# Kernel tuning notes

Hardware: AMD Instinct MI355X
Metric: run time of the kernel (lower is better)

## Reference

```python
import jax, jax.numpy as jnp
import numpy as np

N = 50000
E = 800000
DIM = 256
H = 8
HD = DIM // H


def setup_inputs() -> dict:
    key = jax.random.key(0)
    ks = jax.random.split(key, 8)
    s = 0.02
    return {
        "x": jax.random.normal(ks[0], (N, DIM), jnp.float32),
        "src": jax.random.randint(ks[1], (E,), 0, N, jnp.int32),
        "dst": jax.random.randint(ks[2], (E,), 0, N, jnp.int32),
        "Wqkv": jax.random.normal(ks[3], (DIM, 3 * DIM), jnp.float32) * s,
        "bqkv": jnp.zeros((3 * DIM,), jnp.float32),
        "Wout": jax.random.normal(ks[4], (DIM, DIM), jnp.float32) * s,
        "bout": jnp.zeros((DIM,), jnp.float32),
        "W1": jax.random.normal(ks[5], (2 * DIM, DIM), jnpp := jnp.float32) * s,
        "b1": jnp.zeros((DIM,), jnp.float32),
        "W2": jax.random.normal(ks[6], (DIM, DIM), jnp.float32) * s,
        "b2": jnp.zeros((DIM,), jnp.float32),
    }


def reference(x, src, dst, Wqkv, bqkv, Wout, bout, W1, b1, W2, b2):
    n = x.shape[0]
    scale = 1.0 / np.sqrt(HD).astype(np.float32)
    # QKV projection; torch reshapes [N, 3*dim] -> [N, H, 3*hd] then splits per head
    qkv = (x @ Wqkv + bqkv).reshape(n, H, 3 * HD)
    q, k, v = qkv[..., :HD], qkv[..., HD:2 * HD], qkv[..., 2 * HD:]
    # per-edge attention scores: key at src dotted with query at dst -> [E, H]
    scores = jnp.einsum('ehd,ehd->eh', k[src], q[dst]) * scale
    # edge softmax grouped by destination node
    m = jax.ops.segment_max(scores, dst, num_segments=n)  # [N, H]
    p = jnp.exp(scores - m[dst])
    denom = jax.ops.segment_sum(p, dst, num_segments=n)  # [N, H]
    probs = p / denom[dst]
    # weighted scatter-sum aggregation of source values -> [N, H, HD]
    agg = jax.ops.segment_sum(v[src] * probs[..., None], dst, num_segments=n)
    agg = agg.reshape(n, DIM) @ Wout + bout
    # feed-forward over concat([x, aggregated])
    h = jnp.concatenate([x, agg], axis=1)
    h = jax.nn.gelu(h @ W1 + b1, approximate=False)
    return h @ W2 + b2
```

## Files before the change

kernel.cpp:

```cpp
#include <hip/hip_runtime.h>
#include <hip/hip_bf16.h>
#include <math.h>

#define NDIM 256
#define HDIM 32
#define SCB 512

typedef __attribute__((ext_vector_type(8))) short bf16x8;
typedef __attribute__((ext_vector_type(4))) float f32x4;
typedef __attribute__((ext_vector_type(2))) float f32x2;
typedef unsigned long long ull;

__device__ inline float bf2f(unsigned short u) {
  union { unsigned int i; float f; } c; c.i = ((unsigned int)u) << 16; return c.f;
}
__device__ inline unsigned short f2bf(float f) {
  union { float f; unsigned int i; } c; c.f = f;
  unsigned int x = c.i;
  unsigned int lsb = (x >> 16) & 1u;
  x += 0x7fffu + lsb;
  return (unsigned short)(x >> 16);
}
__device__ inline float4 ldbf4(const unsigned short* p) {
  ull raw = *(const ull*)p;
  float4 f;
  f.x = bf2f((unsigned short)(raw));
  f.y = bf2f((unsigned short)(raw >> 16));
  f.z = bf2f((unsigned short)(raw >> 32));
  f.w = bf2f((unsigned short)(raw >> 48));
  return f;
}
__device__ inline void stbf4(unsigned short* p, float4 v) {
  ull raw = (ull)f2bf(v.x) | ((ull)f2bf(v.y) << 16)
          | ((ull)f2bf(v.z) << 32) | ((ull)f2bf(v.w) << 48);
  *(ull*)p = raw;
}
__device__ inline ull pk4_bf16(float v0, float v1, float v2, float v3) {
  return (ull)f2bf(v0) | ((ull)f2bf(v1) << 16) | ((ull)f2bf(v2) << 32) | ((ull)f2bf(v3) << 48);
}

__device__ inline unsigned char f2e4m3(float v) {
#if __has_builtin(__builtin_amdgcn_cvt_pk_fp8_f32)
  return (unsigned char)(__builtin_amdgcn_cvt_pk_fp8_f32(v, v, 0, false) & 0xff);
#else
  union { float f; unsigned int u; } c; c.f = v;
  unsigned char s = (unsigned char)((c.u >> 24) & 0x80);
  float a = fabsf(v);
  if (!(a < 448.f)) return (unsigned char)(s | 0x7e);
  if (a < 0.0009765625f) return s;
  int e = (int)((c.u >> 23) & 0xff) - 127;
  if (e < -6) {
    int q = (int)rintf(ldexpf(a, 9));
    if (q >= 8) return (unsigned char)(s | 0x08);
    return (unsigned char)(s | q);
  }
  int q = (int)rintf(ldexpf(a, 3 - e));
  if (q == 16) { e++; q = 8; }
  if (e > 8) return (unsigned char)(s | 0x7e);
  return (unsigned char)(s | ((e + 7) << 3) | (q - 8));
#endif
}
__device__ inline unsigned int pk4_e4m3(float v0, float v1, float v2, float v3) {
#if __has_builtin(__builtin_amdgcn_cvt_pk_fp8_f32)
  int w = __builtin_amdgcn_cvt_pk_fp8_f32(v0, v1, 0, false);
  w = __builtin_amdgcn_cvt_pk_fp8_f32(v2, v3, w, true);
  return (unsigned int)w;
#else
  return (unsigned int)f2e4m3(v0) | ((unsigned int)f2e4m3(v1) << 8)
       | ((unsigned int)f2e4m3(v2) << 16) | ((unsigned int)f2e4m3(v3) << 24);
#endif
}
template<bool HI>
__device__ inline f32x2 e4m3pk(unsigned int w) {
#if __has_builtin(__builtin_amdgcn_cvt_pk_f32_fp8)
  return __builtin_amdgcn_cvt_pk_f32_fp8((int)w, HI);
#else
  unsigned int h = HI ? (w >> 16) : w;
  f32x2 r;
  #pragma unroll
  for (int j = 0; j < 2; ++j) {
    unsigned char b = (unsigned char)(h >> (8 * j));
    int e = (b >> 3) & 0xf, mm = b & 7;
    float val = e ? ldexpf((float)(8 + mm), e - 10) : ldexpf((float)mm, -9);
    r[j] = (b & 0x80) ? -val : val;
  }
  return r;
#endif
}

__global__ void fuse0_k(
    const float* __restrict__ x, unsigned short* __restrict__ xb, int n8, int nbx,
    const float* __restrict__ Wqkv, unsigned short* __restrict__ wqkvt,
    const float* __restrict__ W1, unsigned short* __restrict__ wf,
    const float* __restrict__ W2, unsigned short* __restrict__ w2t,
    const float* __restrict__ Wout, const float* __restrict__ bout,
    const float* __restrict__ b1, float* __restrict__ bc, int nbw,
    const int* __restrict__ dst, int* __restrict__ deg, int* __restrict__ erank, int E)
{
  int b = blockIdx.x;
  int tid = threadIdx.x;
  if (b < nbx) {
    int i = b * 256 + tid;
    if (i < n8) {
      const float* p = x + (size_t)i * 8;
      float4 a = *(const float4*)p;
      float4 bv = *(const float4*)(p + 4);
      ull lo = (ull)f2bf(a.x) | ((ull)f2bf(a.y) << 16) | ((ull)f2bf(a.z) << 32) | ((ull)f2bf(a.w) << 48);
      ull hi = (ull)f2bf(bv.x) | ((ull)f2bf(bv.y) << 16) | ((ull)f2bf(bv.z) << 32) | ((ull)f2bf(bv.w) << 48);
      ull* d = (ull*)(xb + (size_t)i * 8);
      d[0] = lo; d[1] = hi;
    }
    return;
  }
  b -= nbx;
  if (b < nbw) {
    int idx = b * 256 + tid;
    if (idx < 196608) {
      int j = idx >> 8, k = idx & 255;
      int seg = j >> 8, jj = j & 255;
      int h = jj >> 5, t = jj & 31;
      int orig = h * 96 + seg * 32 + t;
      wqkvt[(size_t)j * 256 + k] = f2bf(Wqkv[(size_t)k * 768 + orig]);
    } else if (idx < 262144) {
      int i2 = idx - 196608;
      int n = i2 >> 8, k = i2 & 255;
      wf[(size_t)n * 512 + k] = f2bf(W1[(size_t)k * 256 + n]);
    } else if (idx < 327680) {
      int i3 = idx - 262144;
      int n = i3 >> 8, k = i3 & 255;
      w2t[(size_t)n * 256 + k] = f2bf(W2[(size_t)k * 256 + n]);
    } else if (idx < 393216) {
      int i4 = idx - 327680;
      int a = i4 >> 8, n = i4 & 255;
      float s = 0.f;
      #pragma unroll 4
      for (int j = 0; j < 256; ++j)
        s += Wout[(size_t)a * 256 + j] * W1[(size_t)(256 + j) * 256 + n];
      wf[(size_t)n * 512 + 256 + a] = f2bf(s);
    } else if (idx < 393472) {
      int n = idx - 393216;
      float s = b1[n];
      for (int j = 0; j < 256; ++j)
        s += bout[j] * W1[(size_t)(256 + j) * 256 + n];
      bc[n] = s;
    }
    return;
  }
  b -= nbw;
  int e = b * 256 + tid;
  if (e < E) {
    int r = atomicAdd(&deg[dst[e]], 1);
    erank[e] = r;
  }
}

__global__ __launch_bounds__(SCB) void bsum_k(const int* __restrict__ deg, int* __restrict__ bsum, int n) {
  int tid = threadIdx.x;
  int i = blockIdx.x * SCB + tid;
  int v = (i < n) ? deg[i] : 0;
  #pragma unroll
  for (int d = 1; d < 64; d <<= 1) v += __shfl_xor(v, d);
  __shared__ int wsum[8];
  if ((tid & 63) == 0) wsum[tid >> 6] = v;
  __syncthreads();
  if (tid == 0) {
    int s = 0;
    #pragma unroll
    for (int j = 0; j < 8; ++j) s += wsum[j];
    bsum[blockIdx.x] = s;
  }
}

__global__ __launch_bounds__(128) void bscan_k(int* __restrict__ bsum, int nb) {
  __shared__ int tmp[128];
  int tid = threadIdx.x;
  int v = (tid < nb) ? bsum[tid] : 0;
  tmp[tid] = v;
  __syncthreads();
  for (int d = 1; d < 128; d <<= 1) {
    int t = (tid >= d) ? tmp[tid - d] : 0;
    __syncthreads();
    tmp[tid] += t;
    __syncthreads();
  }
  if (tid < nb) bsum[tid] = tmp[tid];
}

__global__ __launch_bounds__(SCB) void offs_k(const int* __restrict__ deg, const int* __restrict__ bsum,
                                              int* __restrict__ offs, int n) {
  int tid = threadIdx.x, lane = tid & 63, wid = tid >> 6;
  int b = blockIdx.x;
  int i = b * SCB + tid;
  int v = (i < n) ? deg[i] : 0;
  int incl = v;
  #pragma unroll
  for (int d = 1; d < 64; d <<= 1) { int t = __shfl_up(incl, d); if (lane >= d) incl += t; }
  __shared__ int wsum[8];
  if (lane == 63) wsum[wid] = incl;
  __syncthreads();
  if (tid < 8) {
    int s = wsum[tid];
    #pragma unroll
    for (int d = 1; d < 8; d <<= 1) { int t = __shfl_up(s, d); if (tid >= d) s += t; }
    wsum[tid] = s;
  }
  __syncthreads();
  int base = (b > 0 ? bsum[b - 1] : 0) + (wid > 0 ? wsum[wid - 1] : 0);
  if (i < n) offs[i] = base + incl - v;
  if (i == n - 1) offs[n] = base + incl;
}

__global__ void scatter2_k(const int* __restrict__ src, const int* __restrict__ dstv,
                           const int* __restrict__ offs, const int* __restrict__ erank,
                           int* __restrict__ ssrc, int E) {
  int e = blockIdx.x * 256 + threadIdx.x;
  if (e < E) ssrc[offs[dstv[e]] + erank[e]] = src[e];
}

__global__ __launch_bounds__(256) void attn_k(
    const unsigned short* Q,
    const unsigned char* __restrict__ K8,
    const unsigned char* __restrict__ V8,
    const int* __restrict__ offs,
    const int* __restrict__ ssrc,
    unsigned short* agg, int N)
{
  int n = blockIdx.x * 4 + (threadIdx.x >> 6);
  if (n >= N) return;
  int lane = threadIdx.x & 63;
  int col = lane << 2;
  const float scale = 0.17677669529663689f;
  float4 q4 = ldbf4(Q + (size_t)n * NDIM + col);
  q4.x *= scale; q4.y *= scale; q4.z *= scale; q4.w *= scale;
  int e0 = offs[n], e1 = offs[n + 1];
  float den = 0.f;
  float ax = 0.f, ay = 0.f, az = 0.f, aw = 0.f;
  int e = e0;
  for (; e + 8 <= e1; e += 8) {
    unsigned int kw[8], vw[8];
    #pragma unroll
    for (int j = 0; j < 8; ++j) {
      int s = ssrc[e + j];
      kw[j] = *(const unsigned int*)(K8 + (size_t)s * NDIM + col);
      vw[j] = *(const unsigned int*)(V8 + (size_t)s * NDIM + col);
    }
    float d[8];
    #pragma unroll
    for (int j = 0; j < 8; ++j) {
      f32x2 k01 = e4m3pk<false>(kw[j]);
      f32x2 k23 = e4m3pk<true>(kw[j]);
      d[j] = q4.x * k01[0] + q4.y * k01[1] + q4.z * k23[0] + q4.w * k23[1];
    }
    #pragma unroll
    for (int j = 0; j < 8; ++j) {
      d[j] += __shfl_xor(d[j], 1);
      d[j] += __shfl_xor(d[j], 2);
      d[j] += __shfl_xor(d[j], 4);
    }
    #pragma unroll
    for (int j = 0; j < 8; ++j) {
      float p = __expf(d[j]);
      den += p;
      f32x2 v01 = e4m3pk<false>(vw[j]);
      f32x2 v23 = e4m3pk<true>(vw[j]);
      ax += p * v01[0]; ay += p * v01[1];
      az += p * v23[0]; aw += p * v23[1];
    }
  }
  for (; e + 4 <= e1; e += 4) {
    unsigned int kw[4], vw[4];
    #pragma unroll
    for (int j = 0; j < 4; ++j) {
      int s = ssrc[e + j];
      kw[j] = *(const unsigned int*)(K8 + (size_t)s * NDIM + col);
      vw[j] = *(const unsigned int*)(V8 + (size_t)s * NDIM + col);
    }
    float d[4];
    #pragma unroll
    for (int j = 0; j < 4; ++j) {
      f32x2 k01 = e4m3pk<false>(kw[j]);
      f32x2 k23 = e4m3pk<true>(kw[j]);
      d[j] = q4.x * k01[0] + q4.y * k01[1] + q4.z * k23[0] + q4.w * k23[1];
    }
    #pragma unroll
    for (int j = 0; j < 4; ++j) {
      d[j] += __shfl_xor(d[j], 1);
      d[j] += __shfl_xor(d[j], 2);
      d[j] += __shfl_xor(d[j], 4);
    }
    #pragma unroll
    for (int j = 0; j < 4; ++j) {
      float p = __expf(d[j]);
      den += p;
      f32x2 v01 = e4m3pk<false>(vw[j]);
      f32x2 v23 = e4m3pk<true>(vw[j]);
      ax += p * v01[0]; ay += p * v01[1];
      az += p * v23[0]; aw += p * v23[1];
    }
  }
  for (; e < e1; ++e) {
    int s = ssrc[e];
    unsigned int kw = *(const unsigned int*)(K8 + (size_t)s * NDIM + col);
    unsigned int vw = *(const unsigned int*)(V8 + (size_t)s * NDIM + col);
    f32x2 k01 = e4m3pk<false>(kw);
    f32x2 k23 = e4m3pk<true>(kw);
    float d = q4.x * k01[0] + q4.y * k01[1] + q4.z * k23[0] + q4.w * k23[1];
    d += __shfl_xor(d, 1);
    d += __shfl_xor(d, 2);
    d += __shfl_xor(d, 4);
    float p = __expf(d);
    den += p;
    f32x2 v01 = e4m3pk<false>(vw);
    f32x2 v23 = e4m3pk<true>(vw);
    ax += p * v01[0]; ay += p * v01[1];
    az += p * v23[0]; aw += p * v23[1];
  }
  float inv = (den > 0.f) ? 1.f / den : 0.f;
  stbf4(agg + (size_t)n * NDIM + col, make_float4(ax * inv, ay * inv, az * inv, aw * inv));
}

__global__ __launch_bounds__(256, 4) void qkv_k(
    const unsigned short* __restrict__ A1, const unsigned short* __restrict__ Wt,
    const float* __restrict__ bias,
    unsigned short* __restrict__ Oq, unsigned char* __restrict__ Ok, unsigned char* __restrict__ Ov,
    int M)
{
  __shared__ char smem[32768];
  unsigned short* As = (unsigned short*)smem;
  unsigned short* Bs = (unsigned short*)(smem + 16384);
  const int tid = threadIdx.x;
  const int lane = tid & 63;
  const int wid = tid >> 6;

  const int nwg = gridDim.x;
  const int q8 = nwg >> 3, r8 = nwg & 7;
  const int xcd = blockIdx.x & 7, idx8 = blockIdx.x >> 3;
  const int swz = (xcd < r8 ? xcd * (q8 + 1) : r8 * (q8 + 1) + (xcd - r8) * q8) + idx8;
  const int nct = 6;
  const int bmt = swz / nct;
  const int bnt = swz - bmt * nct;
  const int bm = bmt * 128;
  const int bn = bnt * 128;

  const int wr = (wid >> 1) << 6;
  const int wc = (wid & 1) << 6;
  const int l15 = lane & 15, lhi = lane >> 4;
  const int srow = lane >> 3;
  const int ssl = (((lane & 7) ^ (lane >> 3)) << 3);

  f32x4 acc[4][4];
  #pragma unroll
  for (int i = 0; i < 4; ++i)
    #pragma unroll
    for (int j = 0; j < 4; ++j) acc[i][j] = (f32x4){0.f, 0.f, 0.f, 0.f};

  for (int k0 = 0; k0 < 256; k0 += 64) {
    #pragma unroll
    for (int t = 0; t < 4; ++t) {
      int qi = wid * 4 + t;
      const unsigned short* ga = A1 + (size_t)(bm + qi * 8 + srow) * 256 + k0 + ssl;
      __builtin_amdgcn_global_load_lds(
          (const __attribute__((address_space(1))) void*)ga,
          (__attribute__((address_space(3))) void*)&As[qi * 512], 16, 0, 0);
      const unsigned short* gb = Wt + (size_t)(bn + qi * 8 + srow) * 256 + k0 + ssl;
      __builtin_amdgcn_global_load_lds(
          (const __attribute__((address_space(1))) void*)gb,
          (__attribute__((address_space(3))) void*)&Bs[qi * 512], 16, 0, 0);
    }
    __syncthreads();
    #pragma unroll
    for (int kk = 0; kk < 64; kk += 32) {
      bf16x8 af[4], bfr[4];
      #pragma unroll
      for (int mi = 0; mi < 4; ++mi) {
        int rA = wr + mi * 16 + l15;
        af[mi] = *(const bf16x8*)&As[rA * 64 + ((((kk >> 3) + lhi) ^ (rA & 7)) << 3)];
      }
      #pragma unroll
      for (int ni = 0; ni < 4; ++ni) {
        int rB = wc + ni * 16 + l15;
        bfr[ni] = *(const bf16x8*)&Bs[rB * 64 + ((((kk >> 3) + lhi) ^ (rB & 7)) << 3)];
      }
      #pragma unroll
      for (int mi = 0; mi < 4; ++mi)
        #pragma unroll
        for (int ni = 0; ni < 4; ++ni)
          acc[mi][ni] = __builtin_amdgcn_mfma_f32_16x16x32_bf16(bfr[ni], af[mi], acc[mi][ni], 0, 0, 0);
    }
    __syncthreads();
  }

  const int seg = (bn + wc) >> 8;
  const int jjbase = (bn + wc) & 255;
  char* slabB = smem + wid * 8192;
  if (seg == 0) {
    #pragma unroll
    for (int ni = 0; ni < 4; ++ni) {
      int cl = ni * 16 + (lhi << 2);
      int jj = jjbase + cl;
      float4 bb = *(const float4*)&bias[(jj >> 5) * 96 + (jj & 31)];
      #pragma unroll
      for (int mi = 0; mi < 4; ++mi) {
        int rl = mi * 16 + l15;
        *(ull*)&slabB[rl * 128 + ((cl * 2) ^ ((rl & 7) << 4))] = pk4_bf16(
            acc[mi][ni][0] + bb.x, acc[mi][ni][1] + bb.y,
            acc[mi][ni][2] + bb.z, acc[mi][ni][3] + bb.w);
      }
    }
    asm volatile("s_waitcnt lgkmcnt(0)" ::: "memory");
    __builtin_amdgcn_sched_barrier(0);
    int rl0 = lane >> 3, co = (lane & 7) << 4;
    #pragma unroll
    for (int t = 0; t < 8; ++t) {
      int rl = t * 8 + rl0;
      int gr = bm + wr + rl;
      if (gr < M)
        *(float4*)&Oq[(size_t)gr * NDIM + jjbase + (co >> 1)] =
            *(float4*)&slabB[rl * 128 + (co ^ ((rl & 7) << 4))];
    }
  } else {
    unsigned char* dstp = (seg == 1) ? Ok : Ov;
    #pragma unroll
    for (int ni = 0; ni < 4; ++ni) {
      int cl = ni * 16 + (lhi << 2);
      int jj = jjbase + cl;
      float4 bb = *(const float4*)&bias[(jj >> 5) * 96 + seg * 32 + (jj & 31)];
      #pragma unroll
      for (int mi = 0; mi < 4; ++mi) {
        int rl = mi * 16 + l15;
        *(unsigned int*)&slabB[rl * 64 + (cl ^ ((rl & 3) << 4))] = pk4_e4m3(
            acc[mi][ni][0] + bb.x, acc[mi][ni][1] + bb.y,
            acc[mi][ni][2] + bb.z, acc[mi][ni][3] + bb.w);
      }
    }
    asm volatile("s_waitcnt lgkmcnt(0)" ::: "memory");
    __builtin_amdgcn_sched_barrier(0);
    int rl0 = lane >> 2, co = (lane & 3) << 4;
    #pragma unroll
    for (int t = 0; t < 4; ++t) {
      int rl = t * 16 + rl0;
      int gr = bm + wr + rl;
      if (gr < M)
        *(float4*)&dstp[(size_t)gr * NDIM + jjbase + co] =
            *(float4*)&slabB[rl * 64 + (co ^ ((rl & 3) << 4))];
    }
  }
}

template<int EPI>
__global__ __launch_bounds__(256, 4) void mgemm_k(
    const unsigned short* __restrict__ A1, const unsigned short* __restrict__ A2,
    const unsigned short* __restrict__ Wt, const float* __restrict__ bias,
    float* __restrict__ Cf, unsigned short* __restrict__ Cb,
    int M, int K1, int K, int Ncol, int ldb, int nct)
{
  __shared__ char smem[32768];
  unsigned short* As = (unsigned short*)smem;
  unsigned short* Bs = (unsigned short*)(smem + 16384);
  const int tid = threadIdx.x;
  const int lane = tid & 63;
  const int wid = tid >> 6;

  const int nwg = gridDim.x;
  const int q8 = nwg >> 3, r8 = nwg & 7;
  const int xcd = blockIdx.x & 7, idx8 = blockIdx.x >> 3;
  const int swz = (xcd < r8 ? xcd * (q8 + 1) : r8 * (q8 + 1) + (xcd - r8) * q8) + idx8;
  const int bmt = swz / nct;
  const int bnt = swz - bmt * nct;
  const int bm = bmt * 128;
  const int bn = bnt * 128;

  const int wr = (wid >> 1) << 6;
  const int wc = (wid & 1) << 6;
  const int l15 = lane & 15, lhi = lane >> 4;
  const int srow = lane >> 3;
  const int ssl = (((lane & 7) ^ (lane >> 3)) << 3);

  f32x4 acc[4][4];
  #pragma unroll
  for (int i = 0; i < 4; ++i)
    #pragma unroll
    for (int j = 0; j < 4; ++j) acc[i][j] = (f32x4){0.f, 0.f, 0.f, 0.f};

  for (int k0 = 0; k0 < K; k0 += 64) {
    const unsigned short* Ab;
    int ks;
    if (k0 < K1) { Ab = A1; ks = k0; } else { Ab = A2; ks = k0 - K1; }
    #pragma unroll
    for (int t = 0; t < 4; ++t) {
      int qi = wid * 4 + t;
      const unsigned short* ga = Ab + (size_t)(bm + qi * 8 + srow) * 256 + ks + ssl;
      __builtin_amdgcn_global_load_lds(
          (const __attribute__((address_space(1))) void*)ga,
          (__attribute__((address_space(3))) void*)&As[qi * 512], 16, 0, 0);
      const unsigned short* gb = Wt + (size_t)(bn + qi * 8 + srow) * ldb + k0 + ssl;
      __builtin_amdgcn_global_load_lds(
          (const __attribute__((address_space(1))) void*)gb,
          (__attribute__((address_space(3))) void*)&Bs[qi * 512], 16, 0, 0);
    }
    __syncthreads();
    #pragma unroll
    for (int kk = 0; kk < 64; kk += 32) {
      bf16x8 af[4], bfr[4];
      #pragma unroll
      for (int mi = 0; mi < 4; ++mi) {
        int rA = wr + mi * 16 + l15;
        af[mi] = *(const bf16x8*)&As[rA * 64 + ((((kk >> 3) + lhi) ^ (rA & 7)) << 3)];
      }
      #pragma unroll
      for (int ni = 0; ni < 4; ++ni) {
        int rB = wc + ni * 16 + l15;
        bfr[ni] = *(const bf16x8*)&Bs[rB * 64 + ((((kk >> 3) + lhi) ^ (rB & 7)) << 3)];
      }
      #pragma unroll
      for (int mi = 0; mi < 4; ++mi)
        #pragma unroll
        for (int ni = 0; ni < 4; ++ni)
          acc[mi][ni] = __builtin_amdgcn_mfma_f32_16x16x32_bf16(bfr[ni], af[mi], acc[mi][ni], 0, 0, 0);
    }
    __syncthreads();
  }

  char* slabB = smem + wid * 8192;
  if (EPI == 0) {
    #pragma unroll
    for (int half = 0; half < 2; ++half) {
      #pragma unroll
      for (int nj = 0; nj < 2; ++nj) {
        int ni = half * 2 + nj;
        int cl = nj * 16 + (lhi << 2);
        float4 bb = *(const float4*)&bias[bn + wc + half * 32 + cl];
        #pragma unroll
        for (int mi = 0; mi < 4; ++mi) {
          int rl = mi * 16 + l15;
          *(float4*)&slabB[rl * 128 + ((cl * 4) ^ ((rl & 7) << 4))] = make_float4(
              acc[mi][ni][0] + bb.x, acc[mi][ni][1] + bb.y,
              acc[mi][ni][2] + bb.z, acc[mi][ni][3] + bb.w);
        }
      }
      asm volatile("s_waitcnt lgkmcnt(0)" ::: "memory");
      __builtin_amdgcn_sched_barrier(0);
      int rl0 = lane >> 3, co = (lane & 7) << 4;
      #pragma unroll
      for (int t = 0; t < 8; ++t) {
        int rl = t * 8 + rl0;
        int gr = bm + wr + rl;
        if (gr < M)
          *(float4*)&Cf[(size_t)gr * Ncol + bn + wc + half * 32 + (co >> 2)] =
              *(float4*)&slabB[rl * 128 + (co ^ ((rl & 7) << 4))];
      }
      if (half == 0) {
        asm volatile("s_waitcnt lgkmcnt(0)" ::: "memory");
        __builtin_amdgcn_sched_barrier(0);
      }
    }
  } else {
    #pragma unroll
    for (int ni = 0; ni < 4; ++ni) {
      int cl = ni * 16 + (lhi << 2);
      float4 bb = *(const float4*)&bias[bn + wc + cl];
      #pragma unroll
      for (int mi = 0; mi < 4; ++mi) {
        int rl = mi * 16 + l15;
        float v0 = acc[mi][ni][0] + bb.x;
        float v1 = acc[mi][ni][1] + bb.y;
        float v2 = acc[mi][ni][2] + bb.z;
        float v3 = acc[mi][ni][3] + bb.w;
        v0 = 0.5f * v0 * (1.0f + erff(v0 * 0.70710678118654752f));
        v1 = 0.5f * v1 * (1.0f + erff(v1 * 0.70710678118654752f));
        v2 = 0.5f * v2 * (1.0f + erff(v2 * 0.70710678118654752f));
        v3 = 0.5f * v3 * (1.0f + erff(v3 * 0.70710678118654752f));
        *(ull*)&slabB[rl * 128 + ((cl * 2) ^ ((rl & 7) << 4))] = pk4_bf16(v0, v1, v2, v3);
      }
    }
    asm volatile("s_waitcnt lgkmcnt(0)" ::: "memory");
    __builtin_amdgcn_sched_barrier(0);
    int rl0 = lane >> 3, co = (lane & 7) << 4;
    #pragma unroll
    for (int t = 0; t < 8; ++t) {
      int rl = t * 8 + rl0;
      int gr = bm + wr + rl;
      if (gr < M)
        *(float4*)&Cb[(size_t)gr * Ncol + bn + wc + (co >> 1)] =
            *(float4*)&slabB[rl * 128 + (co ^ ((rl & 7) << 4))];
    }
  }
}

extern "C" void kernel_launch(void* const* d_in, const int* in_sizes, int n_in,
                              void* d_out, int out_size, void* d_ws, size_t ws_size,
                              hipStream_t stream) {
  (void)n_in; (void)out_size; (void)ws_size;
  const float* x    = (const float*)d_in[0];
  const int*   src  = (const int*)d_in[1];
  const int*   dst  = (const int*)d_in[2];
  const float* Wqkv = (const float*)d_in[3];
  const float* bqkv = (const float*)d_in[4];
  const float* Wout = (const float*)d_in[5];
  const float* bout = (const float*)d_in[6];
  const float* W1   = (const float*)d_in[7];
  const float* b1   = (const float*)d_in[8];
  const float* W2   = (const float*)d_in[9];
  const float* b2   = (const float*)d_in[10];
  float* out = (float*)d_out;

  const int N = in_sizes[0] / NDIM;
  const int E = in_sizes[1];
  const int Mp = (N + 127) & ~127;
  const int nb = (N + SCB - 1) / SCB;

  char* ws = (char*)d_ws;
  size_t off = 0;
  auto alloc = [&](size_t bytes) -> char* {
    char* p = ws + off;
    off += (bytes + 255) & ~(size_t)255;
    return p;
  };
  unsigned short* xb   = (unsigned short*)alloc((size_t)Mp * NDIM * 2);
  unsigned short* Q    = (unsigned short*)alloc((size_t)Mp * NDIM * 2);
  unsigned short* Kb   = (unsigned short*)alloc((size_t)Mp * NDIM * 2);
  unsigned short* Vb   = (unsigned short*)alloc((size_t)Mp * NDIM * 2);
  unsigned short* wqkvt = (unsigned short*)alloc((size_t)768 * 256 * 2);
  unsigned short* wft   = (unsigned short*)alloc((size_t)256 * 512 * 2);
  unsigned short* w2t   = (unsigned short*)alloc((size_t)256 * 256 * 2);
  float*          bc    = (float*)alloc(256 * 4);
  int* deg    = (int*)alloc((size_t)N * 4);
  int* offs   = (int*)alloc((size_t)(N + 1) * 4);
  int* erank  = (int*)alloc((size_t)E * 4);
  int* ssrc   = (int*)alloc((size_t)E * 4);
  int* bsum   = (int*)alloc((size_t)nb * 4);

  unsigned char* K8 = (unsigned char*)Kb;
  unsigned char* V8 = (unsigned char*)Vb;
  unsigned short* agg = Q;
  unsigned short* h1  = Kb;

  const int n8  = N * NDIM / 8;
  const int nbx = (n8 + 255) / 256;
  const int nbw = (393472 + 255) / 256;
  const int nsc = (E + 255) / 256;
  const int mt  = Mp / 128;

  hipMemsetAsync(deg, 0, (size_t)N * 4, stream);

  fuse0_k<<<nbx + nbw + nsc, 256, 0, stream>>>(
      x, xb, n8, nbx, Wqkv, wqkvt, W1, wft, W2, w2t, Wout, bout, b1, bc, nbw,
      dst, deg, erank, E);

  bsum_k<<<nb, SCB, 0, stream>>>(deg, bsum, N);
  bscan_k<<<1, 128, 0, stream>>>(bsum, nb);
  offs_k<<<nb, SCB, 0, stream>>>(deg, bsum, offs, N);

  scatter2_k<<<nsc, 256, 0, stream>>>(src, dst, offs, erank, ssrc, E);

  qkv_k<<<mt * 6, 256, 0, stream>>>(xb, wqkvt, bqkv, Q, K8, V8, N);

  attn_k<<<(N + 3) / 4, 256, 0, stream>>>(Q, K8, V8, offs, ssrc, agg, N);

  mgemm_k<2><<<mt * 2, 256, 0, stream>>>(
      xb, agg, wft, bc, nullptr, h1, N, 256, 512, 256, 512, 2);

  mgemm_k<0><<<mt * 2, 256, 0, stream>>>(
      h1, nullptr, w2t, b2, out, nullptr, N, 256, 256, 256, 256, 2);
}
```

Baseline: 220.8 us.

## Fuse degree histogram into QKV GEMM launch and interleave K/V rows

Moves the edge-degree histogram out of the prep kernel and into the QKV GEMM launch as extra blocks, so the atomic histogram runs alongside the GEMM tiles. K and V fp8 outputs are stored interleaved in one 512-byte row per node, so attention fetches K and V for a source node from the same row. Edge ranks are narrowed to 16-bit to halve that buffer, and the GEMM launch bounds are raised to five waves per SIMD. This risks overflow if any node's in-degree exceeds 65535, and may spill registers under the tighter occupancy bound.

```diff
diff --git a/kernel.cpp b/kernel.cpp
--- a/kernel.cpp
+++ b/kernel.cpp
@@ -3,7 +3,6 @@
 #include <math.h>
 
 #define NDIM 256
-#define HDIM 32
 #define SCB 512
 
 typedef __attribute__((ext_vector_type(8))) short bf16x8;
@@ -88,14 +87,13 @@
 #endif
 }
 
-__global__ void fuse0_k(
+__global__ void prep_k(
     const float* __restrict__ x, unsigned short* __restrict__ xb, int n8, int nbx,
     const float* __restrict__ Wqkv, unsigned short* __restrict__ wqkvt,
     const float* __restrict__ W1, unsigned short* __restrict__ wf,
     const float* __restrict__ W2, unsigned short* __restrict__ w2t,
     const float* __restrict__ Wout, const float* __restrict__ bout,
-    const float* __restrict__ b1, float* __restrict__ bc, int nbw,
-    const int* __restrict__ dst, int* __restrict__ deg, int* __restrict__ erank, int E)
+    const float* __restrict__ b1, float* __restrict__ bc)
 {
   int b = blockIdx.x;
   int tid = threadIdx.x;
@@ -113,44 +111,173 @@
     return;
   }
   b -= nbx;
-  if (b < nbw) {
-    int idx = b * 256 + tid;
-    if (idx < 196608) {
-      int j = idx >> 8, k = idx & 255;
-      int seg = j >> 8, jj = j & 255;
-      int h = jj >> 5, t = jj & 31;
-      int orig = h * 96 + seg * 32 + t;
-      wqkvt[(size_t)j * 256 + k] = f2bf(Wqkv[(size_t)k * 768 + orig]);
-    } else if (idx < 262144) {
-      int i2 = idx - 196608;
-      int n = i2 >> 8, k = i2 & 255;
-      wf[(size_t)n * 512 + k] = f2bf(W1[(size_t)k * 256 + n]);
-    } else if (idx < 327680) {
-      int i3 = idx - 262144;
-      int n = i3 >> 8, k = i3 & 255;
-      w2t[(size_t)n * 256 + k] = f2bf(W2[(size_t)k * 256 + n]);
-    } else if (idx < 393216) {
-      int i4 = idx - 327680;
-      int a = i4 >> 8, n = i4 & 255;
-      float s = 0.f;
-      #pragma unroll 4
-      for (int j = 0; j < 256; ++j)
-        s += Wout[(size_t)a * 256 + j] * W1[(size_t)(256 + j) * 256 + n];
-      wf[(size_t)n * 512 + 256 + a] = f2bf(s);
-    } else if (idx < 393472) {
-      int n = idx - 393216;
-      float s = b1[n];
-      for (int j = 0; j < 256; ++j)
-        s += bout[j] * W1[(size_t)(256 + j) * 256 + n];
-      bc[n] = s;
+  int idx = b * 256 + tid;
+  if (idx < 196608) {
+    int j = idx >> 8, k = idx & 255;
+    int seg = j >> 8, jj = j & 255;
+    int h = jj >> 5, t = jj & 31;
+    int orig = h * 96 + seg * 32 + t;
+    wqkvt[(size_t)j * 256 + k] = f2bf(Wqkv[(size_t)k * 768 + orig]);
+  } else if (idx < 262144) {
+    int i2 = idx - 196608;
+    int n = i2 >> 8, k = i2 & 255;
+    wf[(size_t)n * 512 + k] = f2bf(W1[(size_t)k * 256 + n]);
+  } else if (idx < 327680) {
+    int i3 = idx - 262144;
+    int n = i3 >> 8, k = i3 & 255;
+    w2t[(size_t)n * 256 + k] = f2bf(W2[(size_t)k * 256 + n]);
+  } else if (idx < 393216) {
+    int i4 = idx - 327680;
+    int a = i4 >> 8, n = i4 & 255;
+    float s = 0.f;
+    #pragma unroll 4
+    for (int j = 0; j < 256; ++j)
+      s += Wout[(size_t)a * 256 + j] * W1[(size_t)(256 + j) * 256 + n];
+    wf[(size_t)n * 512 + 256 + a] = f2bf(s);
+  } else if (idx < 393472) {
+    int n = idx - 393216;
+    float s = b1[n];
+    for (int j = 0; j < 256; ++j)
+      s += bout[j] * W1[(size_t)(256 + j) * 256 + n];
+    bc[n] = s;
+  }
+}
+
+__global__ __launch_bounds__(256, 5) void histqkv_k(
+    const int* __restrict__ dstv, int* __restrict__ deg,
+    unsigned short* __restrict__ erank, int E, int nhist,
+    const unsigned short* __restrict__ A1, const unsigned short* __restrict__ Wt,
+    const float* __restrict__ bias,
+    unsigned short* __restrict__ Oq, unsigned char* __restrict__ KV,
+    int M)
+{
+  __shared__ char smem[32768];
+  if (blockIdx.x < nhist) {
+    int e = blockIdx.x * 256 + threadIdx.x;
+    if (e < E) {
+      int r = atomicAdd(&deg[dstv[e]], 1);
+      erank[e] = (unsigned short)r;
     }
     return;
   }
-  b -= nbw;
-  int e = b * 256 + tid;
-  if (e < E) {
-    int r = atomicAdd(&deg[dst[e]], 1);
-    erank[e] = r;
+  unsigned short* As = (unsigned short*)smem;
+  unsigned short* Bs = (unsigned short*)(smem + 16384);
+  const int tid = threadIdx.x;
+  const int lane = tid & 63;
+  const int wid = tid >> 6;
+
+  const int nwg = gridDim.x - nhist;
+  const int bid = blockIdx.x - nhist;
+  const int q8 = nwg >> 3, r8 = nwg & 7;
+  const int xcd = bid & 7, idx8 = bid >> 3;
+  const int swz = (xcd < r8 ? xcd * (q8 + 1) : r8 * (q8 + 1) + (xcd - r8) * q8) + idx8;
+  const int bmt = swz / 6;
+  const int bnt = swz - bmt * 6;
+  const int bm = bmt * 128;
+  const int bn = bnt * 128;
+
+  const int wr = (wid >> 1) << 6;
+  const int wc = (wid & 1) << 6;
+  const int l15 = lane & 15, lhi = lane >> 4;
+  const int srow = lane >> 3;
+  const int ssl = (((lane & 7) ^ (lane >> 3)) << 3);
+
+  f32x4 acc[4][4];
+  #pragma unroll
+  for (int i = 0; i < 4; ++i)
+    #pragma unroll
+    for (int j = 0; j < 4; ++j) acc[i][j] = (f32x4){0.f, 0.f, 0.f, 0.f};
+
+  for (int k0 = 0; k0 < 256; k0 += 64) {
+    #pragma unroll
+    for (int t = 0; t < 4; ++t) {
+      int qi = wid * 4 + t;
+      const unsigned short* ga = A1 + (size_t)(bm + qi * 8 + srow) * 256 + k0 + ssl;
+      __builtin_amdgcn_global_load_lds(
+          (const __attribute__((address_space(1))) void*)ga,
+          (__attribute__((address_space(3))) void*)&As[qi * 512], 16, 0, 0);
+      const unsigned short* gb = Wt + (size_t)(bn + qi * 8 + srow) * 256 + k0 + ssl;
+      __builtin_amdgcn_global_load_lds(
+          (const __attribute__((address_space(1))) void*)gb,
+          (__attribute__((address_space(3))) void*)&Bs[qi * 512], 16, 0, 0);
+    }
+    __syncthreads();
+    #pragma unroll
+    for (int kk = 0; kk < 64; kk += 32) {
+      bf16x8 af[4], bfr[4];
+      #pragma unroll
+      for (int mi = 0; mi < 4; ++mi) {
+        int rA = wr + mi * 16 + l15;
+        af[mi] = *(const bf16x8*)&As[rA * 64 + ((((kk >> 3) + lhi) ^ (rA & 7)) << 3)];
+      }
+      #pragma unroll
+      for (int ni = 0; ni < 4; ++ni) {
+        int rB = wc + ni * 16 + l15;
+        bfr[ni] = *(const bf16x8*)&Bs[rB * 64 + ((((kk >> 3) + lhi) ^ (rB & 7)) << 3)];
+      }
+      #pragma unroll
+      for (int mi = 0; mi < 4; ++mi)
+        #pragma unroll
+        for (int ni = 0; ni < 4; ++ni)
+          acc[mi][ni] = __builtin_amdgcn_mfma_f32_16x16x32_bf16(bfr[ni], af[mi], acc[mi][ni], 0, 0, 0);
+    }
+    __syncthreads();
+  }
+
+  const int seg = (bn + wc) >> 8;
+  const int jjbase = (bn + wc) & 255;
+  char* slabB = smem + wid * 8192;
+  if (seg == 0) {
+    #pragma unroll
+    for (int ni = 0; ni < 4; ++ni) {
+      int cl = ni * 16 + (lhi << 2);
+      int jj = jjbase + cl;
+      float4 bb = *(const float4*)&bias[(jj >> 5) * 96 + (jj & 31)];
+      #pragma unroll
+      for (int mi = 0; mi < 4; ++mi) {
+        int rl = mi * 16 + l15;
+        *(ull*)&slabB[rl * 128 + ((cl * 2) ^ ((rl & 7) << 4))] = pk4_bf16(
+            acc[mi][ni][0] + bb.x, acc[mi][ni][1] + bb.y,
+            acc[mi][ni][2] + bb.z, acc[mi][ni][3] + bb.w);
+      }
+    }
+    asm volatile("s_waitcnt lgkmcnt(0)" ::: "memory");
+    __builtin_amdgcn_sched_barrier(0);
+    int rl0 = lane >> 3, co = (lane & 7) << 4;
+    #pragma unroll
+    for (int t = 0; t < 8; ++t) {
+      int rl = t * 8 + rl0;
+      int gr = bm + wr + rl;
+      if (gr < M)
+        *(float4*)&Oq[(size_t)gr * NDIM + jjbase + (co >> 1)] =
+            *(float4*)&slabB[rl * 128 + (co ^ ((rl & 7) << 4))];
+    }
+  } else {
+    unsigned char* dstp = KV + ((seg == 1) ? 0 : 256);
+    #pragma unroll
+    for (int ni = 0; ni < 4; ++ni) {
+      int cl = ni * 16 + (lhi << 2);
+      int jj = jjbase + cl;
+      float4 bb = *(const float4*)&bias[(jj >> 5) * 96 + seg * 32 + (jj & 31)];
+      #pragma unroll
+      for (int mi = 0; mi < 4; ++mi) {
+        int rl = mi * 16 + l15;
+        *(unsigned int*)&slabB[rl * 64 + (cl ^ ((rl & 3) << 4))] = pk4_e4m3(
+            acc[mi][ni][0] + bb.x, acc[mi][ni][1] + bb.y,
+            acc[mi][ni][2] + bb.z, acc[mi][ni][3] + bb.w);
+      }
+    }
+    asm volatile("s_waitcnt lgkmcnt(0)" ::: "memory");
+    __builtin_amdgcn_sched_barrier(0);
+    int rl0 = lane >> 2, co = (lane & 3) << 4;
+    #pragma unroll
+    for (int t = 0; t < 4; ++t) {
+      int rl = t * 16 + rl0;
+      int gr = bm + wr + rl;
+      if (gr < M)
+        *(float4*)&dstp[(size_t)gr * 512 + jjbase + co] =
+            *(float4*)&slabB[rl * 64 + (co ^ ((rl & 3) << 4))];
+    }
   }
 }
 
@@ -211,7 +338,7 @@
 }
 
 __global__ void scatter2_k(const int* __restrict__ src, const int* __restrict__ dstv,
-                           const int* __restrict__ offs, const int* __restrict__ erank,
+                           const int* __restrict__ offs, const unsigned short* __restrict__ erank,
                            int* __restrict__ ssrc, int E) {
   int e = blockIdx.x * 256 + threadIdx.x;
   if (e < E) ssrc[offs[dstv[e]] + erank[e]] = src[e];
@@ -219,8 +346,7 @@
 
 __global__ __launch_bounds__(256) void attn_k(
     const unsigned short* Q,
-    const unsigned char* __restrict__ K8,
-    const unsigned char* __restrict__ V8,
+    const unsigned char* __restrict__ KV,
     const int* __restrict__ offs,
     const int* __restrict__ ssrc,
     unsigned short* agg, int N)
@@ -241,8 +367,9 @@
     #pragma unroll
     for (int j = 0; j < 8; ++j) {
       int s = ssrc[e + j];
-      kw[j] = *(const unsigned int*)(K8 + (size_t)s * NDIM + col);
-      vw[j] = *(const unsigned int*)(V8 + (size_t)s * NDIM + col);
+      const unsigned char* row = KV + (size_t)s * 512 + col;
+      kw[j] = *(const unsigned int*)row;
+      vw[j] = *(const unsigned int*)(row + 256);
     }
     float d[8];
     #pragma unroll
@@ -272,8 +399,9 @@
     #pragma unroll
     for (int j = 0; j < 4; ++j) {
       int s = ssrc[e + j];
-      kw[j] = *(const unsigned int*)(K8 + (size_t)s * NDIM + col);
-      vw[j] = *(const unsigned int*)(V8 + (size_t)s * NDIM + col);
+      const unsigned char* row = KV + (size_t)s * 512 + col;
+      kw[j] = *(const unsigned int*)row;
+      vw[j] = *(const unsigned int*)(row + 256);
     }
     float d[4];
     #pragma unroll
@@ -300,8 +428,9 @@
   }
   for (; e < e1; ++e) {
     int s = ssrc[e];
-    unsigned int kw = *(const unsigned int*)(K8 + (size_t)s * NDIM + col);
-    unsigned int vw = *(const unsigned int*)(V8 + (size_t)s * NDIM + col);
+    const unsigned char* row = KV + (size_t)s * 512 + col;
+    unsigned int kw = *(const unsigned int*)row;
+    unsigned int vw = *(const unsigned int*)(row + 256);
     f32x2 k01 = e4m3pk<false>(kw);
     f32x2 k23 = e4m3pk<true>(kw);
     float d = q4.x * k01[0] + q4.y * k01[1] + q4.z * k23[0] + q4.w * k23[1];
@@ -319,136 +448,8 @@
   stbf4(agg + (size_t)n * NDIM + col, make_float4(ax * inv, ay * inv, az * inv, aw * inv));
 }
 
-__global__ __launch_bounds__(256, 4) void qkv_k(
-    const unsigned short* __restrict__ A1, const unsigned short* __restrict__ Wt,
-    const float* __restrict__ bias,
-    unsigned short* __restrict__ Oq, unsigned char* __restrict__ Ok, unsigned char* __restrict__ Ov,
-    int M)
-{
-  __shared__ char smem[32768];
-  unsigned short* As = (unsigned short*)smem;
-  unsigned short* Bs = (unsigned short*)(smem + 16384);
-  const int tid = threadIdx.x;
-  const int lane = tid & 63;
-  const int wid = tid >> 6;
-
-  const int nwg = gridDim.x;
-  const int q8 = nwg >> 3, r8 = nwg & 7;
-  const int xcd = blockIdx.x & 7, idx8 = blockIdx.x >> 3;
-  const int swz = (xcd < r8 ? xcd * (q8 + 1) : r8 * (q8 + 1) + (xcd - r8) * q8) + idx8;
-  const int nct = 6;
-  const int bmt = swz / nct;
-  const int bnt = swz - bmt * nct;
-  const int bm = bmt * 128;
-  const int bn = bnt * 128;
-
-  const int wr = (wid >> 1) << 6;
-  const int wc = (wid & 1) << 6;
-  const int l15 = lane & 15, lhi = lane >> 4;
-  const int srow = lane >> 3;
-  const int ssl = (((lane & 7) ^ (lane >> 3)) << 3);
-
-  f32x4 acc[4][4];
-  #pragma unroll
-  for (int i = 0; i < 4; ++i)
-    #pragma unroll
-    for (int j = 0; j < 4; ++j) acc[i][j] = (f32x4){0.f, 0.f, 0.f, 0.f};
-
-  for (int k0 = 0; k0 < 256; k0 += 64) {
-    #pragma unroll
-    for (int t = 0; t < 4; ++t) {
-      int qi = wid * 4 + t;
-      const unsigned short* ga = A1 + (size_t)(bm + qi * 8 + srow) * 256 + k0 + ssl;
-      __builtin_amdgcn_global_load_lds(
-          (const __attribute__((address_space(1))) void*)ga,
-          (__attribute__((address_space(3))) void*)&As[qi * 512], 16, 0, 0);
-      const unsigned short* gb = Wt + (size_t)(bn + qi * 8 + srow) * 256 + k0 + ssl;
-      __builtin_amdgcn_global_load_lds(
-          (const __attribute__((address_space(1))) void*)gb,
-          (__attribute__((address_space(3))) void*)&Bs[qi * 512], 16, 0, 0);
-    }
-    __syncthreads();
-    #pragma unroll
-    for (int kk = 0; kk < 64; kk += 32) {
-      bf16x8 af[4], bfr[4];
-      #pragma unroll
-      for (int mi = 0; mi < 4; ++mi) {
-        int rA = wr + mi * 16 + l15;
-        af[mi] = *(const bf16x8*)&As[rA * 64 + ((((kk >> 3) + lhi) ^ (rA & 7)) << 3)];
-      }
-      #pragma unroll
-      for (int ni = 0; ni < 4; ++ni) {
-        int rB = wc + ni * 16 + l15;
-        bfr[ni] = *(const bf16x8*)&Bs[rB * 64 + ((((kk >> 3) + lhi) ^ (rB & 7)) << 3)];
-      }
-      #pragma unroll
-      for (int mi = 0; mi < 4; ++mi)
-        #pragma unroll
-        for (int ni = 0; ni < 4; ++ni)
-          acc[mi][ni] = __builtin_amdgcn_mfma_f32_16x16x32_bf16(bfr[ni], af[mi], acc[mi][ni], 0, 0, 0);
-    }
-    __syncthreads();
-  }
-
-  const int seg = (bn + wc) >> 8;
-  const int jjbase = (bn + wc) & 255;
-  char* slabB = smem + wid * 8192;
-  if (seg == 0) {
-    #pragma unroll
-    for (int ni = 0; ni < 4; ++ni) {
-      int cl = ni * 16 + (lhi << 2);
-      int jj = jjbase + cl;
-      float4 bb = *(const float4*)&bias[(jj >> 5) * 96 + (jj & 31)];
-      #pragma unroll
-      for (int mi = 0; mi < 4; ++mi) {
-        int rl = mi * 16 + l15;
-        *(ull*)&slabB[rl * 128 + ((cl * 2) ^ ((rl & 7) << 4))] = pk4_bf16(
-            acc[mi][ni][0] + bb.x, acc[mi][ni][1] + bb.y,
-            acc[mi][ni][2] + bb.z, acc[mi][ni][3] + bb.w);
-      }
-    }
-    asm volatile("s_waitcnt lgkmcnt(0)" ::: "memory");
-    __builtin_amdgcn_sched_barrier(0);
-    int rl0 = lane >> 3, co = (lane & 7) << 4;
-    #pragma unroll
-    for (int t = 0; t < 8; ++t) {
-      int rl = t * 8 + rl0;
-      int gr = bm + wr + rl;
-      if (gr < M)
-        *(float4*)&Oq[(size_t)gr * NDIM + jjbase + (co >> 1)] =
-            *(float4*)&slabB[rl * 128 + (co ^ ((rl & 7) << 4))];
-    }
-  } else {
-    unsigned char* dstp = (seg == 1) ? Ok : Ov;
-    #pragma unroll
-    for (int ni = 0; ni < 4; ++ni) {
-      int cl = ni * 16 + (lhi << 2);
-      int jj = jjbase + cl;
-      float4 bb = *(const float4*)&bias[(jj >> 5) * 96 + seg * 32 + (jj & 31)];
-      #pragma unroll
-      for (int mi = 0; mi < 4; ++mi) {
-        int rl = mi * 16 + l15;
-        *(unsigned int*)&slabB[rl * 64 + (cl ^ ((rl & 3) << 4))] = pk4_e4m3(
-            acc[mi][ni][0] + bb.x, acc[mi][ni][1] + bb.y,
-            acc[mi][ni][2] + bb.z, acc[mi][ni][3] + bb.w);
-      }
-    }
-    asm volatile("s_waitcnt lgkmcnt(0)" ::: "memory");
-    __builtin_amdgcn_sched_barrier(0);
-    int rl0 = lane >> 2, co = (lane & 3) << 4;
-    #pragma unroll
-    for (int t = 0; t < 4; ++t) {
-      int rl = t * 16 + rl0;
-      int gr = bm + wr + rl;
-      if (gr < M)
-        *(float4*)&dstp[(size_t)gr * NDIM + jjbase + co] =
-            *(float4*)&slabB[rl * 64 + (co ^ ((rl & 3) << 4))];
-    }
-  }
-}
-
 template<int EPI>
-__global__ __launch_bounds__(256, 4) void mgemm_k(
+__global__ __launch_bounds__(256, 5) void mgemm_k(
     const unsigned short* __restrict__ A1, const unsigned short* __restrict__ A2,
     const unsigned short* __restrict__ Wt, const float* __restrict__ bias,
     float* __restrict__ Cf, unsigned short* __restrict__ Cb,
@@ -618,22 +619,19 @@
   };
   unsigned short* xb   = (unsigned short*)alloc((size_t)Mp * NDIM * 2);
   unsigned short* Q    = (unsigned short*)alloc((size_t)Mp * NDIM * 2);
-  unsigned short* Kb   = (unsigned short*)alloc((size_t)Mp * NDIM * 2);
-  unsigned short* Vb   = (unsigned short*)alloc((size_t)Mp * NDIM * 2);
+  unsigned char*  KV   = (unsigned char*)alloc((size_t)Mp * 512);
+  unsigned short* h1   = (unsigned short*)alloc((size_t)Mp * NDIM * 2);
   unsigned short* wqkvt = (unsigned short*)alloc((size_t)768 * 256 * 2);
   unsigned short* wft   = (unsigned short*)alloc((size_t)256 * 512 * 2);
   unsigned short* w2t   = (unsigned short*)alloc((size_t)256 * 256 * 2);
   float*          bc    = (float*)alloc(256 * 4);
   int* deg    = (int*)alloc((size_t)N * 4);
   int* offs   = (int*)alloc((size_t)(N + 1) * 4);
-  int* erank  = (int*)alloc((size_t)E * 4);
+  unsigned short* erank = (unsigned short*)alloc((size_t)E * 2);
   int* ssrc   = (int*)alloc((size_t)E * 4);
   int* bsum   = (int*)alloc((size_t)nb * 4);
 
-  unsigned char* K8 = (unsigned char*)Kb;
-  unsigned char* V8 = (unsigned char*)Vb;
   unsigned short* agg = Q;
-  unsigned short* h1  = Kb;
 
   const int n8  = N * NDIM / 8;
   const int nbx = (n8 + 255) / 256;
@@ -643,9 +641,12 @@
 
   hipMemsetAsync(deg, 0, (size_t)N * 4, stream);
 
-  fuse0_k<<<nbx + nbw + nsc, 256, 0, stream>>>(
-      x, xb, n8, nbx, Wqkv, wqkvt, W1, wft, W2, w2t, Wout, bout, b1, bc, nbw,
-      dst, deg, erank, E);
+  prep_k<<<nbx + nbw, 256, 0, stream>>>(
+      x, xb, n8, nbx, Wqkv, wqkvt, W1, wft, W2, w2t, Wout, bout, b1, bc);
+
+  histqkv_k<<<nsc + mt * 6, 256, 0, stream>>>(
+      dst, deg, erank, E, nsc,
+      xb, wqkvt, bqkv, Q, KV, N);
 
   bsum_k<<<nb, SCB, 0, stream>>>(deg, bsum, N);
   bscan_k<<<1, 128, 0, stream>>>(bsum, nb);
@@ -653,9 +654,7 @@
 
   scatter2_k<<<nsc, 256, 0, stream>>>(src, dst, offs, erank, ssrc, E);
 
-  qkv_k<<<mt * 6, 256, 0, stream>>>(xb, wqkvt, bqkv, Q, K8, V8, N);
-
-  attn_k<<<(N + 3) / 4, 256, 0, stream>>>(Q, K8, V8, offs, ssrc, agg, N);
+  attn_k<<<(N + 3) / 4, 256, 0, stream>>>(Q, KV, offs, ssrc, agg, N);
 
   mgemm_k<2><<<mt * 2, 256, 0, stream>>>(
       xb, agg, wft, bc, nullptr, h1, N, 256, 512, 256, 512, 2);
```

Result: slower. 305.9 us (+38.5%).
